# Performance work log

Hardware: AMD Instinct MI355X
Metric: run time of the kernel (lower is better)

The kernel has to match this reference:

```python
import jax, jax.numpy as jnp
from jax import lax
import numpy as np

N_PATTS, D_PATTS, L_PATTS = 64, 16, 64
L_OUT = L_PATTS  # module sets l_out = l_patts in both branches
RHO = 0.1
W = RHO ** (1.0 / L_PATTS)  # per-step decay weight
BIG = 1e30  # stands in for +inf at DP boundaries (avoids inf*0 nans)


def _dtw_matrix(x, patts, w):
    """Weighted-DTW DP matrix.
    x: (B, d, T), patts: (P, d, L) -> D: (B, P, L, T)
    D[i,j] = dist[i,j] + w * min(D[i-1,j], D[i,j-1], D[i-1,j-1]),
    with out-of-range predecessors = +inf and D[0,0] = dist[0,0].
    dist is the euclidean distance between x[:, :, j] and patts[:, :, i].
    """
    B, d, T = x.shape
    P, _, L = patts.shape
    x2 = jnp.sum(x * x, axis=1)              # (B, T)
    p2 = jnp.sum(patts * patts, axis=1)      # (P, L)
    xp = jnp.einsum('bdt,pdl->btpl', x, patts)  # (B, T, P, L)
    sq = x2[:, :, None, None] + p2[None, None, :, :] - 2.0 * xp
    dist = jnp.sqrt(jnp.maximum(sq, 1e-12))  # (B, T, P, L)
    dist_t = jnp.transpose(dist, (1, 0, 2, 3))  # (T, B, P, L) scan over time

    def col_step(prev_col, d_col):
        # prev_col = D[:, j-1] of shape (B, P, L); d_col = dist column (B, P, L)
        shifted = jnp.concatenate(
            [jnp.full_like(prev_col[..., :1], BIG), prev_col[..., :-1]], axis=-1)
        c = jnp.minimum(prev_col, shifted)  # min(D[i,j-1], D[i-1,j-1]) per i

        def cell(d_prev, inp):
            dist_i, c_i = inp              # each (B, P)
            m = jnp.minimum(d_prev, c_i)   # min over the 3 predecessors
            val = dist_i + jnp.where(m >= BIG * 0.5, 0.0, w * m)
            return val, val

        init = jnp.full(prev_col.shape[:2], BIG, prev_col.dtype)  # D[-1, j]
        _, col = lax.scan(
            cell, init,
            (jnp.moveaxis(d_col, -1, 0), jnp.moveaxis(c, -1, 0)))  # over i
        col = jnp.moveaxis(col, 0, -1)  # (B, P, L)
        return col, col

    init_col = jnp.full((B, P, L), BIG, dist.dtype)  # D[:, -1] = inf
    _, cols = lax.scan(col_step, init_col, dist_t)   # (T, B, P, L)
    return jnp.transpose(cols, (1, 2, 3, 0))         # (B, P, L, T)


def setup_inputs() -> dict:
    key = jax.random.key(0)
    kx, kp = jax.random.split(key)
    x = jax.random.normal(kx, (16, D_PATTS, 1024), dtype=jnp.float32)
    patts = jax.random.normal(kp, (N_PATTS, D_PATTS, L_PATTS), dtype=jnp.float32)
    return {"x": x, "patts": patts}


def reference(x, patts):
    D = _dtw_matrix(x, patts, W)          # (B, P, L, T)
    return D[:, :, :, -L_OUT:]            # last l_out time steps
```

## Files before the change

kernel.cpp:

```cpp
#include <hip/hip_runtime.h>
#include <math.h>

typedef _Float16 half8 __attribute__((ext_vector_type(8)));
typedef _Float16 h2 __attribute__((ext_vector_type(2)));
typedef float    f32x4 __attribute__((ext_vector_type(4)));
typedef unsigned int u32;
typedef unsigned short u16;

#define BIGV 1e30f

__device__ __forceinline__ u32 dpp_shr1(u32 oldv, u32 src) {
  return (u32)__builtin_amdgcn_update_dpp((int)oldv, (int)src, 0x138, 0xF, 0xF, false);
}
__device__ __forceinline__ float cvtlo(u32 v) {
  union { u16 u; _Float16 h; } c; c.u = (u16)v; return (float)c.h;
}
__device__ __forceinline__ u16 f2h(float f) {
  union { _Float16 h; u16 u; } c; c.h = (_Float16)f; return c.u;
}
__device__ __forceinline__ u32 pkrtz(float a, float b) {
  auto v = __builtin_amdgcn_cvt_pkrtz(a, b);
  union { decltype(v) h; u32 u; } c; c.h = v; return c.u;
}
__device__ __forceinline__ h2 as_h2(u32 u) { union { u32 u; h2 h; } x; x.u = u; return x.h; }

__global__ __launch_bounds__(512) void dtw_pc3(
    const float* __restrict__ x,
    const float* __restrict__ patts,
    float* __restrict__ out,
    float wd) {
  __shared__ uint4 xsq[2050];
  __shared__ u16   x2h16[1024];
  __shared__ uint2 ring2[4 * 64 * 57];

  const int tid = threadIdx.x, lane = tid & 63, wv = tid >> 6;
  const int b = blockIdx.x >> 4, pg = blockIdx.x & 15;
  const int role = wv >> 2, pr = wv & 3;
  const int p = pg * 4 + pr;
  const int le = lane & 15, kq = lane >> 4;

  {
    const float* xb = x + b * (16 * 1024);
    u16* xh = (u16*)xsq;
    for (int idx = tid; idx < 16384; idx += 512) {
      int d = idx >> 10, t = idx & 1023;
      xh[t * 16 + d] = f2h(xb[idx]);
    }
    if (tid == 0) { xsq[2048] = make_uint4(0,0,0,0); xsq[2049] = make_uint4(0,0,0,0); }
    __syncthreads();
    for (int t = tid; t < 1024; t += 512) {
      uint4 a0 = xsq[2 * t], a1 = xsq[2 * t + 1];
      float s2 = __builtin_amdgcn_fdot2(as_h2(a0.x), as_h2(a0.x), 0.f, false);
      s2 = __builtin_amdgcn_fdot2(as_h2(a0.y), as_h2(a0.y), s2, false);
      s2 = __builtin_amdgcn_fdot2(as_h2(a0.z), as_h2(a0.z), s2, false);
      s2 = __builtin_amdgcn_fdot2(as_h2(a0.w), as_h2(a0.w), s2, false);
      s2 = __builtin_amdgcn_fdot2(as_h2(a1.x), as_h2(a1.x), s2, false);
      s2 = __builtin_amdgcn_fdot2(as_h2(a1.y), as_h2(a1.y), s2, false);
      s2 = __builtin_amdgcn_fdot2(as_h2(a1.z), as_h2(a1.z), s2, false);
      s2 = __builtin_amdgcn_fdot2(as_h2(a1.w), as_h2(a1.w), s2, false);
      x2h16[t] = f2h(s2);
    }
  }
  __syncthreads();

  if (role == 0) {
    half8 bf[4];
    {
      const float* pp = patts + p * (16 * 64);
#pragma unroll
      for (int nb = 0; nb < 4; ++nb) {
        float pv[8]; float part = 0.f;
#pragma unroll
        for (int j = 0; j < 8; ++j) {
          float f = (kq < 2) ? pp[(8 * kq + j) * 64 + nb * 16 + le] : 0.f;
          pv[j] = f; part = fmaf(f, f, part);
        }
        part += __shfl_xor(part, 16, 64);
        part += __shfl_xor(part, 32, 64);
        u32 wd0 = pkrtz(-2.f * pv[0], -2.f * pv[1]);
        u32 wd1 = pkrtz(-2.f * pv[2], -2.f * pv[3]);
        u32 wd2 = pkrtz(-2.f * pv[4], -2.f * pv[5]);
        u32 wd3 = pkrtz(-2.f * pv[6], -2.f * pv[7]);
        if (kq == 2) { wd0 = 0x3C00u | ((u32)f2h(part) << 16); wd1 = 0; wd2 = 0; wd3 = 0; }
        union { uint4 q; half8 h; } bu; bu.q = make_uint4(wd0, wd1, wd2, wd3);
        bf[nb] = bu.h;
      }
    }
    u32 Aa[4], Ee[4];
    const u32 pairbase = (u32)(pr * 29184);
#pragma unroll
    for (int nb = 0; nb < 4; ++nb) {
      int row = nb * 16 + le;
      u32 rb = pairbase + (u32)(row * 456);
      Aa[nb] = rb + (u32)(4 * (2 * kq + (row & ~1)));
      Ee[nb] = rb + 448u;
    }

#define PRODUCE(T0) { \
    int aidx_ = (kq < 2) ? (2 * ((T0) + le) + kq) : 2048; \
    uint4 aq_ = xsq[aidx_]; \
    u32 x2b_ = (u32)x2h16[(T0) + le]; \
    aq_.x = (kq == 2) ? (x2b_ | 0x3C000000u) : aq_.x; \
    union { uint4 q; half8 h; } au_; au_.q = aq_; \
    _Pragma("unroll") \
    for (int nb_ = 0; nb_ < 4; ++nb_) { \
      f32x4 c_ = {0.f, 0.f, 0.f, 0.f}; \
      c_ = __builtin_amdgcn_mfma_f32_16x16x32_f16(au_.h, bf[nb_], c_, 0, 0, 0); \
      float d0_ = __builtin_amdgcn_sqrtf(fmaxf(c_[0], 1e-12f)); \
      float d1_ = __builtin_amdgcn_sqrtf(fmaxf(c_[1], 1e-12f)); \
      float d2_ = __builtin_amdgcn_sqrtf(fmaxf(c_[2], 1e-12f)); \
      float d3_ = __builtin_amdgcn_sqrtf(fmaxf(c_[3], 1e-12f)); \
      uint2 st_; st_.x = pkrtz(d0_, d1_); st_.y = pkrtz(d2_, d3_); \
      *(uint2*)((char*)ring2 + Aa[nb_]) = st_; \
      Aa[nb_] += 32u; if (Aa[nb_] >= Ee[nb_]) Aa[nb_] -= 448u; \
    } }

    PRODUCE(0); PRODUCE(16); PRODUCE(32); PRODUCE(48);
    __syncthreads();
#pragma unroll 1
    for (int k = 0; k < 30; ++k) {
      PRODUCE(32 * k + 64);
      PRODUCE(32 * k + 80);
      __syncthreads();
    }
    for (int k = 0; k < 6; ++k) __syncthreads();

  } else {
    char* crow = (char*)ring2 + pr * 29184 + lane * 456;
    u32 cb = 0;
    const bool oddl = (lane & 1) != 0;
    float prevB = BIGV, sA = BIGV, sB = BIGV, sBo = BIGV;
    const int bigbits = __float_as_int(BIGV);
    float* oprow = out + ((b * 64 + p) * 64 + lane) * 64;
    float* ps = oprow;
    uint2 C0,C1,C2,C3,C4,C5,C6,C7, N0,N1,N2,N3,N4,N5,N6,N7;
    uint2 carry; carry.x = 0; carry.y = 0;

#define DPSTEP(K, WRD, PM, EP) { \
    u32 wrd_ = (WRD); \
    float d0_ = cvtlo(wrd_); float d1_ = cvtlo(wrd_ >> 16); \
    float mA_ = fminf(fminf(prevB, sA), sBo); \
    if (PM) mA_ = (mA_ >= 0.5e30f) ? 0.f : mA_; \
    float vA_ = fmaf(wd, mA_, d0_); \
    float mB_ = fminf(fminf(vA_, sB), sA); \
    float vB_ = fmaf(wd, mB_, d1_); \
    if (PM) { bool act_ = ((K) >= lane); vA_ = act_ ? vA_ : BIGV; vB_ = act_ ? vB_ : BIGV; } \
    if (EP) { if ((u32)((K) - lane - 480) < 32u) \
        *(float2*)(ps + 2 * ((K) & 15)) = make_float2(vA_, vB_); } \
    sBo = sB; \
    sA = __int_as_float((int)dpp_shr1((u32)bigbits, (u32)__float_as_int(vA_))); \
    sB = __int_as_float((int)dpp_shr1((u32)bigbits, (u32)__float_as_int(vB_))); \
    prevB = vB_; }

#define PAIR2(K2, CJ, CJM1, PM, EP) { \
    u32 w0_ = oddl ? (CJM1).y : (CJ).x; \
    u32 w1_ = oddl ? (CJ).x   : (CJ).y; \
    DPSTEP((K2),     w0_, PM, EP); \
    DPSTEP((K2) + 1, w1_, PM, EP); }

#define CLOAD(Q0,Q1,Q2,Q3,Q4,Q5,Q6,Q7) { \
    char* na_ = crow + cb; \
    Q0 = *(uint2*)(na_);      Q1 = *(uint2*)(na_ + 8); \
    Q2 = *(uint2*)(na_ + 16); Q3 = *(uint2*)(na_ + 24); \
    Q4 = *(uint2*)(na_ + 32); Q5 = *(uint2*)(na_ + 40); \
    Q6 = *(uint2*)(na_ + 48); Q7 = *(uint2*)(na_ + 56); \
    cb += 64; if (cb == 448) cb = 0; }

#define PHASE(A0_,A1_,A2_,A3_,A4_,A5_,A6_,A7_, B0_,B1_,B2_,B3_,B4_,B5_,B6_,B7_, K0, PM, EP) { \
    if (EP) ps = oprow + (2 * (K0) - 960) - 2 * lane; \
    CLOAD(B0_,B1_,B2_,B3_,B4_,B5_,B6_,B7_); \
    PAIR2((K0) + 0,  A0_, carry, PM, EP); \
    PAIR2((K0) + 2,  A1_, A0_,   PM, EP); \
    PAIR2((K0) + 4,  A2_, A1_,   PM, EP); \
    PAIR2((K0) + 6,  A3_, A2_,   PM, EP); \
    PAIR2((K0) + 8,  A4_, A3_,   PM, EP); \
    PAIR2((K0) + 10, A5_, A4_,   PM, EP); \
    PAIR2((K0) + 12, A6_, A5_,   PM, EP); \
    PAIR2((K0) + 14, A7_, A6_,   PM, EP); \
    carry = A7_; \
    __builtin_amdgcn_s_barrier(); }

    __builtin_amdgcn_s_barrier();
    CLOAD(C0,C1,C2,C3,C4,C5,C6,C7);

    PHASE(C0,C1,C2,C3,C4,C5,C6,C7, N0,N1,N2,N3,N4,N5,N6,N7, 0,  1, 0);
    PHASE(N0,N1,N2,N3,N4,N5,N6,N7, C0,C1,C2,C3,C4,C5,C6,C7, 16, 1, 0);
    PHASE(C0,C1,C2,C3,C4,C5,C6,C7, N0,N1,N2,N3,N4,N5,N6,N7, 32, 1, 0);
    PHASE(N0,N1,N2,N3,N4,N5,N6,N7, C0,C1,C2,C3,C4,C5,C6,C7, 48, 1, 0);
#pragma unroll 1
    for (int j = 2; j < 15; ++j) {
      PHASE(C0,C1,C2,C3,C4,C5,C6,C7, N0,N1,N2,N3,N4,N5,N6,N7, 32 * j,      0, 0);
      PHASE(N0,N1,N2,N3,N4,N5,N6,N7, C0,C1,C2,C3,C4,C5,C6,C7, 32 * j + 16, 0, 0);
    }
    PHASE(C0,C1,C2,C3,C4,C5,C6,C7, N0,N1,N2,N3,N4,N5,N6,N7, 480, 0, 1);
    PHASE(N0,N1,N2,N3,N4,N5,N6,N7, C0,C1,C2,C3,C4,C5,C6,C7, 496, 0, 1);
    PHASE(C0,C1,C2,C3,C4,C5,C6,C7, N0,N1,N2,N3,N4,N5,N6,N7, 512, 0, 1);
    PHASE(N0,N1,N2,N3,N4,N5,N6,N7, C0,C1,C2,C3,C4,C5,C6,C7, 528, 0, 1);
    PHASE(C0,C1,C2,C3,C4,C5,C6,C7, N0,N1,N2,N3,N4,N5,N6,N7, 544, 0, 1);
    PHASE(N0,N1,N2,N3,N4,N5,N6,N7, C0,C1,C2,C3,C4,C5,C6,C7, 560, 0, 1);
  }
}

extern "C" void kernel_launch(void* const* d_in, const int* in_sizes, int n_in,
                              void* d_out, int out_size, void* d_ws, size_t ws_size,
                              hipStream_t stream) {
  const float* x     = (const float*)d_in[0];
  const float* patts = (const float*)d_in[1];
  float* out         = (float*)d_out;
  const float w = (float)exp(log(0.1) / 64.0);
  dim3 grid(256), block(512);
  hipLaunchKernelGGL(dtw_pc3, grid, block, 0, stream, x, patts, out, w);
}
```

Before: 44.26 us.

## Switch DTW wavefront to single-cell skewed diagonals with column-major dist ring

Measured after the change: 45.59 us. 1.03x slower.

```diff
diff --git a/kernel.cpp b/kernel.cpp
--- a/kernel.cpp
+++ b/kernel.cpp
@@ -8,6 +8,9 @@
 typedef unsigned short u16;
 
 #define BIGV 1e30f
+#define RQ   57
+#define ROWB 456
+#define PAIRB (64 * ROWB)
 
 __device__ __forceinline__ u32 dpp_shr1(u32 oldv, u32 src) {
   return (u32)__builtin_amdgcn_update_dpp((int)oldv, (int)src, 0x138, 0xF, 0xF, false);
@@ -24,14 +27,14 @@
 }
 __device__ __forceinline__ h2 as_h2(u32 u) { union { u32 u; h2 h; } x; x.u = u; return x.h; }
 
-__global__ __launch_bounds__(512) void dtw_pc3(
+__global__ __launch_bounds__(512) void dtw_sg(
     const float* __restrict__ x,
     const float* __restrict__ patts,
     float* __restrict__ out,
     float wd) {
   __shared__ uint4 xsq[2050];
   __shared__ u16   x2h16[1024];
-  __shared__ uint2 ring2[4 * 64 * 57];
+  __shared__ uint2 ring2[4 * 64 * RQ];
 
   const int tid = threadIdx.x, lane = tid & 63, wv = tid >> 6;
   const int b = blockIdx.x >> 4, pg = blockIdx.x & 15;
@@ -86,15 +89,8 @@
         bf[nb] = bu.h;
       }
     }
-    u32 Aa[4], Ee[4];
-    const u32 pairbase = (u32)(pr * 29184);
-#pragma unroll
-    for (int nb = 0; nb < 4; ++nb) {
-      int row = nb * 16 + le;
-      u32 rb = pairbase + (u32)(row * 456);
-      Aa[nb] = rb + (u32)(4 * (2 * kq + (row & ~1)));
-      Ee[nb] = rb + 448u;
-    }
+    int colp = 8 * kq;
+    const int wpbase = pr * (64 * RQ) + RQ * le;
 
 #define PRODUCE(T0) { \
     int aidx_ = (kq < 2) ? (2 * ((T0) + le) + kq) : 2048; \
@@ -102,6 +98,7 @@
     u32 x2b_ = (u32)x2h16[(T0) + le]; \
     aq_.x = (kq == 2) ? (x2b_ | 0x3C000000u) : aq_.x; \
     union { uint4 q; half8 h; } au_; au_.q = aq_; \
+    int wb_ = wpbase + (colp >> 3); \
     _Pragma("unroll") \
     for (int nb_ = 0; nb_ < 4; ++nb_) { \
       f32x4 c_ = {0.f, 0.f, 0.f, 0.f}; \
@@ -111,9 +108,9 @@
       float d2_ = __builtin_amdgcn_sqrtf(fmaxf(c_[2], 1e-12f)); \
       float d3_ = __builtin_amdgcn_sqrtf(fmaxf(c_[3], 1e-12f)); \
       uint2 st_; st_.x = pkrtz(d0_, d1_); st_.y = pkrtz(d2_, d3_); \
-      *(uint2*)((char*)ring2 + Aa[nb_]) = st_; \
-      Aa[nb_] += 32u; if (Aa[nb_] >= Ee[nb_]) Aa[nb_] -= 448u; \
-    } }
+      ring2[wb_ + 16 * RQ * nb_] = st_; \
+    } \
+    colp += 32; if (colp >= 448) colp -= 448; }
 
     PRODUCE(0); PRODUCE(16); PRODUCE(32); PRODUCE(48);
     __syncthreads();
@@ -126,78 +123,78 @@
     for (int k = 0; k < 6; ++k) __syncthreads();
 
   } else {
-    char* crow = (char*)ring2 + pr * 29184 + lane * 456;
-    u32 cb = 0;
-    const bool oddl = (lane & 1) != 0;
-    float prevB = BIGV, sA = BIGV, sB = BIGV, sBo = BIGV;
+    const char* crow = (const char*)ring2 + pr * PAIRB + lane * ROWB;
+    const int  l2 = 2 * lane;
+    u32 byte0 = (u32)((448 - 4 * lane) % 448);
+    u32 colc  = byte0 & ~7u;
+    const bool sel2 = (lane & 1) != 0;
     const int bigbits = __float_as_int(BIGV);
+    float prev = BIGV, q1 = BIGV, q2 = BIGV, q3 = BIGV, pend = 0.f;
     float* oprow = out + ((b * 64 + p) * 64 + lane) * 64;
-    float* ps = oprow;
-    uint2 C0,C1,C2,C3,C4,C5,C6,C7, N0,N1,N2,N3,N4,N5,N6,N7;
-    uint2 carry; carry.x = 0; carry.y = 0;
-
-#define DPSTEP(K, WRD, PM, EP) { \
-    u32 wrd_ = (WRD); \
-    float d0_ = cvtlo(wrd_); float d1_ = cvtlo(wrd_ >> 16); \
-    float mA_ = fminf(fminf(prevB, sA), sBo); \
-    if (PM) mA_ = (mA_ >= 0.5e30f) ? 0.f : mA_; \
-    float vA_ = fmaf(wd, mA_, d0_); \
-    float mB_ = fminf(fminf(vA_, sB), sA); \
-    float vB_ = fmaf(wd, mB_, d1_); \
-    if (PM) { bool act_ = ((K) >= lane); vA_ = act_ ? vA_ : BIGV; vB_ = act_ ? vB_ : BIGV; } \
-    if (EP) { if ((u32)((K) - lane - 480) < 32u) \
-        *(float2*)(ps + 2 * ((K) & 15)) = make_float2(vA_, vB_); } \
-    sBo = sB; \
-    sA = __int_as_float((int)dpp_shr1((u32)bigbits, (u32)__float_as_int(vA_))); \
-    sB = __int_as_float((int)dpp_shr1((u32)bigbits, (u32)__float_as_int(vB_))); \
-    prevB = vB_; }
-
-#define PAIR2(K2, CJ, CJM1, PM, EP) { \
-    u32 w0_ = oddl ? (CJM1).y : (CJ).x; \
-    u32 w1_ = oddl ? (CJ).x   : (CJ).y; \
-    DPSTEP((K2),     w0_, PM, EP); \
-    DPSTEP((K2) + 1, w1_, PM, EP); }
-
-#define CLOAD(Q0,Q1,Q2,Q3,Q4,Q5,Q6,Q7) { \
-    char* na_ = crow + cb; \
-    Q0 = *(uint2*)(na_);      Q1 = *(uint2*)(na_ + 8); \
-    Q2 = *(uint2*)(na_ + 16); Q3 = *(uint2*)(na_ + 24); \
-    Q4 = *(uint2*)(na_ + 32); Q5 = *(uint2*)(na_ + 40); \
-    Q6 = *(uint2*)(na_ + 48); Q7 = *(uint2*)(na_ + 56); \
-    cb += 64; if (cb == 448) cb = 0; }
-
-#define PHASE(A0_,A1_,A2_,A3_,A4_,A5_,A6_,A7_, B0_,B1_,B2_,B3_,B4_,B5_,B6_,B7_, K0, PM, EP) { \
-    if (EP) ps = oprow + (2 * (K0) - 960) - 2 * lane; \
-    CLOAD(B0_,B1_,B2_,B3_,B4_,B5_,B6_,B7_); \
-    PAIR2((K0) + 0,  A0_, carry, PM, EP); \
-    PAIR2((K0) + 2,  A1_, A0_,   PM, EP); \
-    PAIR2((K0) + 4,  A2_, A1_,   PM, EP); \
-    PAIR2((K0) + 6,  A3_, A2_,   PM, EP); \
-    PAIR2((K0) + 8,  A4_, A3_,   PM, EP); \
-    PAIR2((K0) + 10, A5_, A4_,   PM, EP); \
-    PAIR2((K0) + 12, A6_, A5_,   PM, EP); \
-    PAIR2((K0) + 14, A7_, A6_,   PM, EP); \
-    carry = A7_; \
+
+#define WRAP448(X) ((X) >= 448u ? (X) - 448u : (X))
+#define LQ(DST, OFF) { u32 o_ = WRAP448((u32)(OFF)); DST = *(const uint2*)(crow + o_); }
+
+#define DPS(S, D, MODE) { \
+    float dist_ = (D); \
+    float m_ = fminf(fminf(prev, q2), q3); \
+    if ((MODE) == 0) m_ = (m_ >= 0.5e30f) ? 0.f : m_; \
+    float val_ = fmaf(wd, m_, dist_); \
+    float cur_ = val_; \
+    if ((MODE) == 0) cur_ = ((S) >= l2) ? val_ : BIGV; \
+    if ((MODE) == 3) cur_ = (l2 >= (S) - 1023) ? val_ : BIGV; \
+    if ((MODE) >= 2) { \
+      if (((S) & 1) == 0) { pend = val_; } \
+      else { int t_ = (S) - l2; if ((u32)(t_ - 961) < 63u) \
+        *(float2*)(oprow + (t_ - 961)) = make_float2(pend, val_); } \
+    } \
+    q3 = q2; q2 = q1; \
+    q1 = __int_as_float((int)dpp_shr1((u32)bigbits, (u32)__float_as_int(cur_))); \
+    prev = cur_; }
+
+#define G16(G0, G1, G2, G3, G4, S0, MODE) { \
+    u32 w0 = sel2 ? G0.y : G0.x, w1 = sel2 ? G1.x : G0.y; \
+    u32 w2 = sel2 ? G1.y : G1.x, w3 = sel2 ? G2.x : G1.y; \
+    u32 w4 = sel2 ? G2.y : G2.x, w5 = sel2 ? G3.x : G2.y; \
+    u32 w6 = sel2 ? G3.y : G3.x, w7 = sel2 ? G4.x : G3.y; \
+    DPS((S0)+0,  cvtlo(w0), MODE); DPS((S0)+1,  cvtlo(w0 >> 16), MODE); \
+    DPS((S0)+2,  cvtlo(w1), MODE); DPS((S0)+3,  cvtlo(w1 >> 16), MODE); \
+    DPS((S0)+4,  cvtlo(w2), MODE); DPS((S0)+5,  cvtlo(w2 >> 16), MODE); \
+    DPS((S0)+6,  cvtlo(w3), MODE); DPS((S0)+7,  cvtlo(w3 >> 16), MODE); \
+    DPS((S0)+8,  cvtlo(w4), MODE); DPS((S0)+9,  cvtlo(w4 >> 16), MODE); \
+    DPS((S0)+10, cvtlo(w5), MODE); DPS((S0)+11, cvtlo(w5 >> 16), MODE); \
+    DPS((S0)+12, cvtlo(w6), MODE); DPS((S0)+13, cvtlo(w6 >> 16), MODE); \
+    DPS((S0)+14, cvtlo(w7), MODE); DPS((S0)+15, cvtlo(w7 >> 16), MODE); }
+
+#define PHASE9(C0,C1,C2,C3,C4,C5,C6,C7, D8, N1,N2,N3,N4,N5,N6,N7, S0, MODE) { \
+    LQ(D8, colc + 64); \
+    G16(C0, C1, C2, C3, C4, S0, MODE); \
+    LQ(N1, colc + 72);  LQ(N2, colc + 80);  LQ(N3, colc + 88); \
+    LQ(N4, colc + 96);  LQ(N5, colc + 104); LQ(N6, colc + 112); LQ(N7, colc + 120); \
+    G16(C4, C5, C6, C7, D8, (S0) + 16, MODE); \
+    colc = WRAP448(colc + 64); \
     __builtin_amdgcn_s_barrier(); }
 
     __builtin_amdgcn_s_barrier();
-    CLOAD(C0,C1,C2,C3,C4,C5,C6,C7);
-
-    PHASE(C0,C1,C2,C3,C4,C5,C6,C7, N0,N1,N2,N3,N4,N5,N6,N7, 0,  1, 0);
-    PHASE(N0,N1,N2,N3,N4,N5,N6,N7, C0,C1,C2,C3,C4,C5,C6,C7, 16, 1, 0);
-    PHASE(C0,C1,C2,C3,C4,C5,C6,C7, N0,N1,N2,N3,N4,N5,N6,N7, 32, 1, 0);
-    PHASE(N0,N1,N2,N3,N4,N5,N6,N7, C0,C1,C2,C3,C4,C5,C6,C7, 48, 1, 0);
+    uint2 a0,a1,a2,a3,a4,a5,a6,a7,a8, b0,b1,b2,b3,b4,b5,b6,b7;
+    LQ(a0, colc + 0);  LQ(a1, colc + 8);  LQ(a2, colc + 16); LQ(a3, colc + 24);
+    LQ(a4, colc + 32); LQ(a5, colc + 40); LQ(a6, colc + 48); LQ(a7, colc + 56);
+
+    PHASE9(a0,a1,a2,a3,a4,a5,a6,a7, a8, b1,b2,b3,b4,b5,b6,b7, 0,  0);
+    PHASE9(a8,b1,b2,b3,b4,b5,b6,b7, b0, a1,a2,a3,a4,a5,a6,a7, 32, 0);
+    PHASE9(b0,a1,a2,a3,a4,a5,a6,a7, a8, b1,b2,b3,b4,b5,b6,b7, 64, 0);
+    PHASE9(a8,b1,b2,b3,b4,b5,b6,b7, b0, a1,a2,a3,a4,a5,a6,a7, 96, 0);
 #pragma unroll 1
-    for (int j = 2; j < 15; ++j) {
-      PHASE(C0,C1,C2,C3,C4,C5,C6,C7, N0,N1,N2,N3,N4,N5,N6,N7, 32 * j,      0, 0);
-      PHASE(N0,N1,N2,N3,N4,N5,N6,N7, C0,C1,C2,C3,C4,C5,C6,C7, 32 * j + 16, 0, 0);
-    }
-    PHASE(C0,C1,C2,C3,C4,C5,C6,C7, N0,N1,N2,N3,N4,N5,N6,N7, 480, 0, 1);
-    PHASE(N0,N1,N2,N3,N4,N5,N6,N7, C0,C1,C2,C3,C4,C5,C6,C7, 496, 0, 1);
-    PHASE(C0,C1,C2,C3,C4,C5,C6,C7, N0,N1,N2,N3,N4,N5,N6,N7, 512, 0, 1);
-    PHASE(N0,N1,N2,N3,N4,N5,N6,N7, C0,C1,C2,C3,C4,C5,C6,C7, 528, 0, 1);
-    PHASE(C0,C1,C2,C3,C4,C5,C6,C7, N0,N1,N2,N3,N4,N5,N6,N7, 544, 0, 1);
-    PHASE(N0,N1,N2,N3,N4,N5,N6,N7, C0,C1,C2,C3,C4,C5,C6,C7, 560, 0, 1);
+    for (int j = 0; j < 13; ++j) {
+      PHASE9(b0,a1,a2,a3,a4,a5,a6,a7, a8, b1,b2,b3,b4,b5,b6,b7, 0, 1);
+      PHASE9(a8,b1,b2,b3,b4,b5,b6,b7, b0, a1,a2,a3,a4,a5,a6,a7, 0, 1);
+    }
+    PHASE9(b0,a1,a2,a3,a4,a5,a6,a7, a8, b1,b2,b3,b4,b5,b6,b7, 960,  2);
+    PHASE9(a8,b1,b2,b3,b4,b5,b6,b7, b0, a1,a2,a3,a4,a5,a6,a7, 992,  2);
+    PHASE9(b0,a1,a2,a3,a4,a5,a6,a7, a8, b1,b2,b3,b4,b5,b6,b7, 1024, 3);
+    PHASE9(a8,b1,b2,b3,b4,b5,b6,b7, b0, a1,a2,a3,a4,a5,a6,a7, 1056, 3);
+    PHASE9(b0,a1,a2,a3,a4,a5,a6,a7, a8, b1,b2,b3,b4,b5,b6,b7, 1088, 3);
+    PHASE9(a8,b1,b2,b3,b4,b5,b6,b7, b0, a1,a2,a3,a4,a5,a6,a7, 1120, 3);
   }
 }
 
@@ -209,5 +206,5 @@
   float* out         = (float*)d_out;
   const float w = (float)exp(log(0.1) / 64.0);
   dim3 grid(256), block(512);
-  hipLaunchKernelGGL(dtw_pc3, grid, block, 0, stream, x, patts, out, w);
-}
+  hipLaunchKernelGGL(dtw_sg, grid, block, 0, stream, x, patts, out, w);
+}
```
